# Kernel optimization log

Measured on AMD Instinct MI355X. Metric: run time of the kernel, lower is better.

## Reference

```python
import jax, jax.numpy as jnp
import numpy as np

HEADS = 8
LN_EPS = 1e-5
BN_EPS = 1e-5
MIN_EPS, MAX_EPS = 1e-4, 10.0


def _ln(x, g, b):
    m = x.mean(-1, keepdims=True)
    v = x.var(-1, keepdims=True)
    return (x - m) / jnp.sqrt(v + LN_EPS) * g + b


def _pos2d(a, b, dim, temperature=10000.0):
    # faithful to build_2d_sincos_position_embedding(w=a, h=b)
    grid_a = jnp.arange(a, dtype=jnp.float32)
    grid_b = jnp.arange(b, dtype=jnp.float32)
    ga, gb = jnp.meshgrid(grid_a, grid_b, indexing='ij')  # (a, b)
    pos_dim = dim // 4
    omega = 1.0 / (temperature ** (jnp.arange(pos_dim, dtype=jnp.float32) / pos_dim))
    out_a = ga.flatten()[:, None] * omega[None]
    out_b = gb.flatten()[:, None] * omega[None]
    return jnp.concatenate([jnp.sin(out_a), jnp.cos(out_a), jnp.sin(out_b), jnp.cos(out_b)], axis=1)  # (a*b, dim)


def _avgpool(x, k):
    bb, cc, H, W = x.shape
    return x.reshape(bb, cc, H // k, k, W // k, k).mean((3, 5))


def setup_inputs() -> dict:
    key = jax.random.key(0)
    c1, c2, bs = 256, 512, 16
    ks = jax.random.split(key, 12)

    def lin(k, o, i):
        return (jax.random.normal(k, (o, i), jnp.float32) * (1.0 / np.sqrt(i))).astype(jnp.float32)

    return {
        'a3': jax.random.normal(ks[0], (bs, c1, 80, 80), jnp.float32),
        'a4': jax.random.normal(ks[1], (bs, c2, 40, 40), jnp.float32),
        'conv_w': lin(ks[2], c1, c2), 'conv_b': jnp.zeros((c1,), jnp.float32),
        'bn_g': jnp.ones((c1,), jnp.float32), 'bn_b': jnp.zeros((c1,), jnp.float32),
        'q_w': lin(ks[3], c1, c1), 'q_b': jnp.zeros((c1,), jnp.float32),
        'q_ln_g': jnp.ones((c1,), jnp.float32), 'q_ln_b': jnp.zeros((c1,), jnp.float32),
        'k_w': lin(ks[4], c1, c1), 'k_b': jnp.zeros((c1,), jnp.float32),
        'k_ln_g': jnp.ones((c1,), jnp.float32), 'k_ln_b': jnp.zeros((c1,), jnp.float32),
        'v_w': lin(ks[5], c1, c1), 'v_b': jnp.zeros((c1,), jnp.float32),
        'out_w': lin(ks[6], c1, c1), 'out_b': jnp.zeros((c1,), jnp.float32),
        'lin1_w': lin(ks[7], 4 * c1, c1), 'lin1_b': jnp.zeros((4 * c1,), jnp.float32),
        'lin2_w': lin(ks[8], c1, 4 * c1), 'lin2_b': jnp.zeros((c1,), jnp.float32),
        'norm1_g': jnp.ones((c1,), jnp.float32), 'norm1_b': jnp.zeros((c1,), jnp.float32),
        'norm2_g': jnp.ones((c1,), jnp.float32), 'norm2_b': jnp.zeros((c1,), jnp.float32),
        'idx': 10,
    }


def reference(a3, a4, conv_w, conv_b, bn_g, bn_b, q_w, q_b, q_ln_g, q_ln_b,
              k_w, k_b, k_ln_g, k_ln_b, v_w, v_b, out_w, out_b,
              lin1_w, lin1_b, lin2_w, lin2_b, norm1_g, norm1_b, norm2_g, norm2_b, idx):
    a3 = jnp.nan_to_num(a3, nan=0.0, posinf=1e4, neginf=-1e4)
    a4 = jnp.nan_to_num(a4, nan=0.0, posinf=1e4, neginf=-1e4)
    orig_a3, orig_a4 = a3, a4

    # high_to_low_embed: 1x1 conv + BatchNorm (eval: running_mean=0, running_var=1)
    a4e = jnp.einsum('bchw,oc->bohw', a4, conv_w) + conv_b[None, :, None, None]
    a4e = a4e / jnp.sqrt(1.0 + BN_EPS) * bn_g[None, :, None, None] + bn_b[None, :, None, None]

    if idx == 10:
        a3d = _avgpool(a3, 2)
    else:
        a3d = _avgpool(a3, 4)
        a4e = _avgpool(a4e, 2)

    bs, c, h, w = a3d.shape
    tgt = h * w
    src = a4e.shape[2] * a4e.shape[3]

    residual = a3d.reshape(bs, c, tgt).transpose(0, 2, 1)      # (bs, tgt, c)
    a3f = a3d.reshape(bs, c, tgt).transpose(2, 0, 1)            # (tgt, bs, c)
    a4f = a4e.reshape(bs, c, src).transpose(2, 0, 1)            # (src, bs, c)

    pos = _pos2d(h, w, c)[:, None, :]                           # (h*w, 1, c)
    a3f = a3f + pos
    a4f = a4f + pos                                             # src == tgt by construction

    Q = jax.nn.relu(_ln(a3f @ q_w.T + q_b, q_ln_g, q_ln_b))
    K = jax.nn.relu(_ln(a4f @ k_w.T + k_b, k_ln_g, k_ln_b))
    V = a4f @ v_w.T + v_b

    hd = c // HEADS
    Q = Q.reshape(tgt, bs, HEADS, hd).transpose(1, 2, 0, 3)     # (b, h, tgt, hd)
    K = K.reshape(src, bs, HEADS, hd).transpose(1, 2, 0, 3)
    V = V.reshape(src, bs, HEADS, hd).transpose(1, 2, 0, 3)

    m = max(src, tgt)
    wi = (np.pi / 2) * jnp.arange(1, m + 1, dtype=jnp.float32) / m  # (m,)
    sq = jnp.sin(wi[:tgt])[None, None, :, None]
    cq = jnp.cos(wi[:tgt])[None, None, :, None]
    sk = jnp.sin(wi[:src])[None, None, :, None]
    ck = jnp.cos(wi[:src])[None, None, :, None]
    Q_ = jnp.concatenate([Q * sq, Q * cq], -1)                  # (b, h, tgt, 2hd)
    K_ = jnp.concatenate([K * sk, K * ck], -1)                  # (b, h, src, 2hd)

    KV = jnp.einsum('bhsd,bhse->bhde', K_, V)                   # (b, h, 2hd, hd)
    Zden = jnp.einsum('bhld,bhd->bhl', Q_, K_.sum(2))
    Z = 1.0 / jnp.clip(Zden, MIN_EPS, MAX_EPS)
    attn = jnp.einsum('bhld,bhde->bhle', Q_, KV) * Z[..., None]  # (b, h, tgt, hd)

    attn = attn.transpose(2, 0, 1, 3).reshape(tgt, bs, c)
    out = (attn @ out_w.T + out_b).transpose(1, 0, 2)           # (bs, tgt, c)
    out = _ln(out, norm1_g, norm1_b)
    out = residual + out

    res2 = out
    ff = jax.nn.gelu(out @ lin1_w.T + lin1_b, approximate=False) @ lin2_w.T + lin2_b
    ff = _ln(ff, norm2_g, norm2_b)
    out = res2 + ff

    a3_sa = out.transpose(0, 2, 1).reshape(bs, c, h, w)
    a3_sa = jax.image.resize(a3_sa, orig_a3.shape, 'bilinear')  # align_corners=False
    a3_sa = a3_sa * orig_a3

    B4, C4, H4, W4 = orig_a4.shape
    a4_up = jax.image.resize(orig_a4, (B4, C4, 2 * H4, 2 * W4), 'bilinear')
    return (a3_sa, a4_up)
```

## Files before the change

### kernel.cpp

```cpp
#include <hip/hip_runtime.h>
#include <math.h>


typedef __attribute__((ext_vector_type(8))) short bf16x8;
typedef __attribute__((ext_vector_type(8))) unsigned short us8;
typedef __attribute__((ext_vector_type(4))) unsigned short us4h;
typedef __attribute__((ext_vector_type(4))) float f32x4;

__device__ __forceinline__ unsigned short f2bf(float f) {
  unsigned int u = __float_as_uint(f);
  u += 0x7fff + ((u >> 16) & 1);
  return (unsigned short)(u >> 16);
}
__device__ __forceinline__ float bf2f(unsigned short u) {
  return __uint_as_float(((unsigned int)u) << 16);
}

__global__ __launch_bounds__(256) void wprep_kernel(
    const float* __restrict__ cw, const float* __restrict__ qw,
    const float* __restrict__ kw, const float* __restrict__ vw,
    const float* __restrict__ ow, const float* __restrict__ l1w,
    const float* __restrict__ l2w, unsigned short* __restrict__ wbf) {
  int gid = blockIdx.x * 256 + threadIdx.x;
  size_t e0 = (size_t)gid * 8;
  const float* src; size_t off;
  if (e0 < 131072)      { src = cw;  off = e0; }
  else if (e0 < 196608) { src = qw;  off = e0 - 131072; }
  else if (e0 < 262144) { src = kw;  off = e0 - 196608; }
  else if (e0 < 327680) { src = vw;  off = e0 - 262144; }
  else if (e0 < 393216) { src = ow;  off = e0 - 327680; }
  else if (e0 < 655360) { src = l1w; off = e0 - 393216; }
  else                  { src = l2w; off = e0 - 655360; }
  float4 v0 = *(const float4*)(src + off);
  float4 v1 = *(const float4*)(src + off + 4);
  us8 r;
  r[0] = f2bf(v0.x); r[1] = f2bf(v0.y); r[2] = f2bf(v0.z); r[3] = f2bf(v0.w);
  r[4] = f2bf(v1.x); r[5] = f2bf(v1.y); r[6] = f2bf(v1.z); r[7] = f2bf(v1.w);
  *(us8*)(wbf + e0) = r;
}

__global__ void pos_kernel(float* __restrict__ pos) {
  int s = blockIdx.x, c = threadIdx.x;
  int y = s / 40, x = s - y * 40;
  int quad = c >> 6, i = c & 63;
  float omega = expf(-(float)i * (9.2103403719761836f / 64.0f));
  float coord = (quad < 2) ? (float)y : (float)x;
  float a = coord * omega;
  pos[s * 256 + c] = (quad & 1) ? cosf(a) : sinf(a);
}

__global__ __launch_bounds__(640) void avgpool_kernel(
    const float* __restrict__ a3, const float* __restrict__ pos,
    unsigned short* __restrict__ X3) {
  __shared__ float buf2[256][44];
  int y = blockIdx.x, b = blockIdx.y;
  int tid = threadIdx.x;
  int x2 = tid % 20, cq = tid / 20;
#pragma unroll
  for (int it = 0; it < 8; ++it) {
    int c = cq + 32 * it;
    const float* p = a3 + (((size_t)(b * 256 + c) * 80 + 2 * y) * 80 + x2 * 4);
    float4 r0 = *(const float4*)p;
    float4 r1 = *(const float4*)(p + 80);
    buf2[c][2 * x2]     = 0.25f * ((r0.x + r0.y) + (r1.x + r1.y));
    buf2[c][2 * x2 + 1] = 0.25f * ((r0.z + r0.w) + (r1.z + r1.w));
  }
  __syncthreads();
  size_t t0 = (size_t)b * 1600 + y * 40;
  int sbase = y * 40;
#pragma unroll
  for (int it = 0; it < 4; ++it) {
    int idx = it * 640 + tid;
    int c = idx & 255, xq = idx >> 8;
    int x0 = xq * 4;
    float4 v = *(const float4*)&buf2[c][x0];
#pragma unroll
    for (int j = 0; j < 4; ++j) {
      float pv = pos[(size_t)(sbase + x0 + j) * 256 + c];
      float vv = (j == 0) ? v.x : (j == 1) ? v.y : (j == 2) ? v.z : v.w;
      X3[(t0 + x0 + j) * 256 + c] = f2bf(vv + pv);
    }
  }
}

__global__ __launch_bounds__(256) void a4t_kernel(
    const float* __restrict__ a4, unsigned short* __restrict__ a4t) {
  __shared__ float buf[64][65];
  int s0 = blockIdx.x * 64, k0 = blockIdx.y * 64, b = blockIdx.z;
  const float* src = a4 + ((size_t)b * 512 + k0) * 1600 + s0;
#pragma unroll
  for (int p = 0; p < 4; ++p) {
    int idx = p * 256 + threadIdx.x;
    int kk = idx >> 4, s4 = (idx & 15) * 4;
    float4 v = *(const float4*)(src + (size_t)kk * 1600 + s4);
    buf[kk][s4 + 0] = v.x; buf[kk][s4 + 1] = v.y;
    buf[kk][s4 + 2] = v.z; buf[kk][s4 + 3] = v.w;
  }
  __syncthreads();
  unsigned short* dst = a4t + ((size_t)b * 1600 + s0) * 512 + k0;
#pragma unroll
  for (int p = 0; p < 4; ++p) {
    int idx = p * 256 + threadIdx.x;
    int ss = idx >> 4, kq = (idx & 15) * 4;
    us4h v;
    v[0] = f2bf(buf[kq + 0][ss]); v[1] = f2bf(buf[kq + 1][ss]);
    v[2] = f2bf(buf[kq + 2][ss]); v[3] = f2bf(buf[kq + 3][ss]);
    *(us4h*)(dst + (size_t)ss * 512 + kq) = v;
  }
}

template<int EPI>
__global__ __launch_bounds__(256) void fgemm(
    const unsigned short* __restrict__ A, const unsigned short* __restrict__ W,
    const float* __restrict__ bias, void* __restrict__ outp,
    const int K, const int ldN,
    const float* __restrict__ posb,
    const float* __restrict__ g1, const float* __restrict__ b1,
    const unsigned short* __restrict__ res) {
  __shared__ __align__(16) unsigned short Albs[64][40];
  __shared__ __align__(16) unsigned short Wlds[256][40];
  __shared__ float part[2][64][2];
  int tid = threadIdx.x;
  int lane = tid & 63, w = tid >> 6;
  int m0 = (w >> 1) * 32, n0 = (w & 1) * 128;
  int g = lane >> 4, cl = lane & 15;
  int t0 = blockIdx.x * 64, o0 = blockIdx.y * 256;
  f32x4 acc[2][8] = {};
  int arr = tid >> 2, acol = (tid & 3) * 8;

  for (int k0 = 0; k0 < K; k0 += 32) {
    __syncthreads();
    *(us8*)&Albs[arr][acol] = *(const us8*)(A + (size_t)(t0 + arr) * K + (k0 + acol));
#pragma unroll
    for (int p = 0; p < 4; ++p) {
      int idx = p * 256 + tid;
      int rr = idx >> 2, cc = (idx & 3) * 8;
      *(us8*)&Wlds[rr][cc] = *(const us8*)(W + (size_t)(o0 + rr) * K + (k0 + cc));
    }
    __syncthreads();
    bf16x8 af[2], bw[8];
#pragma unroll
    for (int ms = 0; ms < 2; ++ms)
      af[ms] = *(const bf16x8*)&Albs[m0 + ms * 16 + cl][g * 8];
#pragma unroll
    for (int ns = 0; ns < 8; ++ns)
      bw[ns] = *(const bf16x8*)&Wlds[n0 + ns * 16 + cl][g * 8];
#pragma unroll
    for (int ms = 0; ms < 2; ++ms)
#pragma unroll
      for (int ns = 0; ns < 8; ++ns)
        acc[ms][ns] = __builtin_amdgcn_mfma_f32_16x16x32_bf16(af[ms], bw[ns], acc[ms][ns], 0, 0, 0);
  }

  float bv[8];
#pragma unroll
  for (int ns = 0; ns < 8; ++ns) bv[ns] = bias[o0 + n0 + ns * 16 + cl];
  int sbase = t0 % 1600;

  if constexpr (EPI == 2 || EPI == 3 || EPI == 5) {
#pragma unroll
    for (int ms = 0; ms < 2; ++ms) {
#pragma unroll
      for (int i = 0; i < 4; ++i) {
        float p = 0.f, q = 0.f;
#pragma unroll
        for (int ns = 0; ns < 8; ++ns) {
          float v = acc[ms][ns][i] + bv[ns];
          p += v; q += v * v;
        }
        p += __shfl_xor(p, 1); q += __shfl_xor(q, 1);
        p += __shfl_xor(p, 2); q += __shfl_xor(q, 2);
        p += __shfl_xor(p, 4); q += __shfl_xor(q, 4);
        p += __shfl_xor(p, 8); q += __shfl_xor(q, 8);
        if (cl == 0) {
          int rl = m0 + ms * 16 + g * 4 + i;
          part[w & 1][rl][0] = p;
          part[w & 1][rl][1] = q;
        }
      }
    }
    __syncthreads();
  }

  unsigned short* ob = (unsigned short*)outp;
  float* of = (float*)outp;
#pragma unroll
  for (int ms = 0; ms < 2; ++ms) {
#pragma unroll
    for (int i = 0; i < 4; ++i) {
      int rl = m0 + ms * 16 + g * 4 + i;
      int t = t0 + rl;
      float mean = 0.f, inv = 0.f;
      if constexpr (EPI == 2 || EPI == 3 || EPI == 5) {
        float sp = part[0][rl][0] + part[1][rl][0];
        float sq = part[0][rl][1] + part[1][rl][1];
        mean = sp * (1.f / 256.f);
        float var = sq * (1.f / 256.f) - mean * mean;
        inv = rsqrtf(var + 1e-5f);
      }
#pragma unroll
      for (int ns = 0; ns < 8; ++ns) {
        int col = n0 + ns * 16 + cl;
        float v = acc[ms][ns][i] + bv[ns];
        size_t oidx = (size_t)t * ldN + o0 + col;
        if constexpr (EPI == 0) {
          ob[oidx] = f2bf(v);
        } else if constexpr (EPI == 1) {
          const float is = 0.99999500003749968f;
          float y = v * (is * g1[col]) + b1[col] + posb[(size_t)(sbase + rl) * 256 + col];
          ob[oidx] = f2bf(y);
        } else if constexpr (EPI == 2) {
          float y = (v - mean) * inv * g1[col] + b1[col];
          ob[oidx] = f2bf(fmaxf(y, 0.f));
        } else if constexpr (EPI == 3) {
          float y = (v - mean) * inv * g1[col] + b1[col];
          y += bf2f(res[(size_t)t * 256 + col]) - posb[(size_t)(sbase + rl) * 256 + col];
          ob[oidx] = f2bf(y);
        } else if constexpr (EPI == 4) {
          float y = 0.5f * v * (1.f + erff(v * 0.7071067811865475f));
          ob[oidx] = f2bf(y);
        } else {
          float y = (v - mean) * inv * g1[col] + b1[col];
          y += bf2f(res[(size_t)t * 256 + col]);
          of[oidx] = y;
        }
      }
    }
  }
}

__global__ __launch_bounds__(256) void kv_kernel(
    const unsigned short* __restrict__ Kb, const unsigned short* __restrict__ Vb,
    float* __restrict__ KVp, float* __restrict__ Ksp) {
  __shared__ float Kc[64][32];
  __shared__ float Vc[64][32];
  __shared__ float sv[64], cv[64];
  __shared__ float red[4][64];
  int bx = blockIdx.x;
  int bh = bx / 5, sp = bx - bh * 5;
  int b = bh >> 3, h = bh & 7;
  int tid = threadIdx.x;
  int e = tid & 31, dg = tid >> 5;
  int d4 = dg * 4;
  int dks = tid & 63, partid = tid >> 6;
  float accs[4] = {0.f, 0.f, 0.f, 0.f};
  float accc[4] = {0.f, 0.f, 0.f, 0.f};
  float ks = 0.f;
  size_t base = ((size_t)b * 1600) * 256 + h * 32;
  for (int s0 = sp * 320; s0 < sp * 320 + 320; s0 += 64) {
    __syncthreads();
#pragma unroll
    for (int p = 0; p < 8; ++p) {
      int si = dg + p * 8;
      Kc[si][e] = bf2f(Kb[base + (size_t)(s0 + si) * 256 + e]);
      Vc[si][e] = bf2f(Vb[base + (size_t)(s0 + si) * 256 + e]);
    }
    if (tid < 64) {
      float wv = 1.5707963267948966f * (float)(s0 + tid + 1) * (1.0f / 1600.0f);
      sv[tid] = sinf(wv);
      cv[tid] = cosf(wv);
    }
    __syncthreads();
#pragma unroll 8
    for (int si = 0; si < 64; ++si) {
      float vv = Vc[si][e];
      float sn = sv[si], cs = cv[si];
      float4 k4 = *(const float4*)&Kc[si][d4];
      float p0 = k4.x * vv, p1 = k4.y * vv, p2 = k4.z * vv, p3 = k4.w * vv;
      accs[0] = fmaf(p0, sn, accs[0]); accc[0] = fmaf(p0, cs, accc[0]);
      accs[1] = fmaf(p1, sn, accs[1]); accc[1] = fmaf(p1, cs, accc[1]);
      accs[2] = fmaf(p2, sn, accs[2]); accc[2] = fmaf(p2, cs, accc[2]);
      accs[3] = fmaf(p3, sn, accs[3]); accc[3] = fmaf(p3, cs, accc[3]);
    }
#pragma unroll 4
    for (int q = 0; q < 16; ++q) {
      int si = partid * 16 + q;
      float kvv = (dks < 32) ? Kc[si][dks] * sv[si] : Kc[si][dks - 32] * cv[si];
      ks += kvv;
    }
  }
  red[partid][dks] = ks;
  __syncthreads();
  size_t ob = (size_t)sp * 128 + bh;
  if (tid < 64)
    Ksp[ob * 64 + tid] = (red[0][tid] + red[1][tid]) + (red[2][tid] + red[3][tid]);
#pragma unroll
  for (int i = 0; i < 4; ++i) {
    KVp[ob * 2048 + (d4 + i) * 32 + e] = accs[i];
    KVp[ob * 2048 + (32 + d4 + i) * 32 + e] = accc[i];
  }
}

__global__ __launch_bounds__(256) void kvred_kernel(
    const float* __restrict__ KVp, const float* __restrict__ Ksp,
    float* __restrict__ KV, float* __restrict__ Ks) {
  int bh = blockIdx.x, tid = threadIdx.x;
  size_t o = (size_t)bh * 2048 + tid * 8;
  float4 s0 = make_float4(0, 0, 0, 0), s1 = make_float4(0, 0, 0, 0);
#pragma unroll
  for (int sp = 0; sp < 5; ++sp) {
    const float* p = KVp + ((size_t)sp * 128 + bh) * 2048 + tid * 8;
    float4 a = *(const float4*)p;
    float4 b2 = *(const float4*)(p + 4);
    s0.x += a.x; s0.y += a.y; s0.z += a.z; s0.w += a.w;
    s1.x += b2.x; s1.y += b2.y; s1.z += b2.z; s1.w += b2.w;
  }
  *(float4*)(KV + o) = s0;
  *(float4*)(KV + o + 4) = s1;
  if (tid < 64) {
    float t = 0.f;
#pragma unroll
    for (int sp = 0; sp < 5; ++sp) t += Ksp[((size_t)sp * 128 + bh) * 64 + tid];
    Ks[bh * 64 + tid] = t;
  }
}

__global__ __launch_bounds__(256) void attn_kernel(
    const unsigned short* __restrict__ Qb, const float* __restrict__ KV,
    const float* __restrict__ Ksum, unsigned short* __restrict__ attn) {
  int grp = threadIdx.x >> 5;
  int e = threadIdx.x & 31;
  int t = blockIdx.x * 8 + grp;
  int b = t / 1600, s = t - b * 1600;
  float wv = 1.5707963267948966f * (float)(s + 1) * (1.0f / 1600.0f);
  float sq = sinf(wv), cq = cosf(wv);
  const unsigned short* qrow = Qb + (size_t)t * 256;
  for (int h = 0; h < 8; ++h) {
    int bh = b * 8 + h;
    const float* kv = KV + (size_t)bh * 2048;
    const float* ksm = Ksum + (size_t)bh * 64;
    float qe = bf2f(qrow[h * 32 + e]);
    float zp = qe * (sq * ksm[e] + cq * ksm[32 + e]);
    zp += __shfl_xor(zp, 1); zp += __shfl_xor(zp, 2);
    zp += __shfl_xor(zp, 4); zp += __shfl_xor(zp, 8); zp += __shfl_xor(zp, 16);
    float acc = 0.f;
#pragma unroll 8
    for (int d = 0; d < 32; ++d) {
      float qv = bf2f(qrow[h * 32 + d]);
      acc = fmaf(qv * sq, kv[d * 32 + e], acc);
      acc = fmaf(qv * cq, kv[(32 + d) * 32 + e], acc);
    }
    float zc = fminf(fmaxf(zp, 1e-4f), 10.0f);
    attn[(size_t)t * 256 + h * 32 + e] = f2bf(acc * (1.0f / zc));
  }
}

__global__ __launch_bounds__(256) void transpose_kernel(
    const float* __restrict__ X, float* __restrict__ Y) {
  __shared__ float buf[40 * 257];
  int y = blockIdx.x, b = blockIdx.y;
  int tid = threadIdx.x;
  size_t t0 = (size_t)b * 1600 + y * 40;
  for (int it = 0; it < 40; ++it)
    buf[it * 257 + tid] = X[(t0 + it) * 256 + tid];
  __syncthreads();
  for (int it = 0; it < 40; ++it) {
    int idx = it * 256 + tid;
    int c = idx / 40, x = idx - c * 40;
    Y[((size_t)(b * 256 + c) * 1600) + y * 40 + x] = buf[x * 257 + c];
  }
}

__device__ __forceinline__ float bilin40(const float* sm, int Y, int X) {
  float fy = Y * 0.5f - 0.25f;
  int iy = (int)floorf(fy);
  float dy = fy - (float)iy;
  int y0 = iy < 0 ? 0 : iy;
  int y1 = (iy + 1) > 39 ? 39 : (iy + 1);
  float fx = X * 0.5f - 0.25f;
  int ix = (int)floorf(fx);
  float dx = fx - (float)ix;
  int x0 = ix < 0 ? 0 : ix;
  int x1 = (ix + 1) > 39 ? 39 : (ix + 1);
  float v00 = sm[y0 * 40 + x0], v01 = sm[y0 * 40 + x1];
  float v10 = sm[y1 * 40 + x0], v11 = sm[y1 * 40 + x1];
  return (1.f - dy) * ((1.f - dx) * v00 + dx * v01) +
         dy * ((1.f - dx) * v10 + dx * v11);
}

__global__ __launch_bounds__(256) void upsample_mul_kernel(
    const float* __restrict__ src, const float* __restrict__ a3, float* __restrict__ out) {
  __shared__ float sm[1600];
  int c = blockIdx.x, b = blockIdx.y;
  size_t sbase = ((size_t)b * 256 + c) * 1600;
  for (int i = threadIdx.x; i < 1600; i += 256) sm[i] = src[sbase + i];
  __syncthreads();
  size_t obase = ((size_t)b * 256 + c) * 6400;
  for (int it = 0; it < 25; ++it) {
    int idx = it * 256 + threadIdx.x;
    int Y = idx / 80, X = idx - Y * 80;
    out[obase + idx] = bilin40(sm, Y, X) * a3[obase + idx];
  }
}

__global__ __launch_bounds__(256) void upsample_kernel(
    const float* __restrict__ src, float* __restrict__ out) {
  __shared__ float sm[1600];
  int c = blockIdx.x, b = blockIdx.y;
  size_t sbase = ((size_t)b * 512 + c) * 1600;
  for (int i = threadIdx.x; i < 1600; i += 256) sm[i] = src[sbase + i];
  __syncthreads();
  size_t obase = ((size_t)b * 512 + c) * 6400;
  for (int it = 0; it < 25; ++it) {
    int idx = it * 256 + threadIdx.x;
    int Y = idx / 80, X = idx - Y * 80;
    out[obase + idx] = bilin40(sm, Y, X);
  }
}

extern "C" void kernel_launch(void* const* d_in, const int* in_sizes, int n_in,
                              void* d_out, int out_size, void* d_ws, size_t ws_size,
                              hipStream_t stream) {
  const float* a3     = (const float*)d_in[0];
  const float* a4     = (const float*)d_in[1];
  const float* conv_w = (const float*)d_in[2];
  const float* conv_b = (const float*)d_in[3];
  const float* bn_g   = (const float*)d_in[4];
  const float* bn_b   = (const float*)d_in[5];
  const float* q_w    = (const float*)d_in[6];
  const float* q_b    = (const float*)d_in[7];
  const float* q_ln_g = (const float*)d_in[8];
  const float* q_ln_b = (const float*)d_in[9];
  const float* k_w    = (const float*)d_in[10];
  const float* k_b    = (const float*)d_in[11];
  const float* k_ln_g = (const float*)d_in[12];
  const float* k_ln_b = (const float*)d_in[13];
  const float* v_w    = (const float*)d_in[14];
  const float* v_b    = (const float*)d_in[15];
  const float* out_w  = (const float*)d_in[16];
  const float* out_b  = (const float*)d_in[17];
  const float* lin1_w = (const float*)d_in[18];
  const float* lin1_b = (const float*)d_in[19];
  const float* lin2_w = (const float*)d_in[20];
  const float* lin2_b = (const float*)d_in[21];
  const float* n1_g   = (const float*)d_in[22];
  const float* n1_b   = (const float*)d_in[23];
  const float* n2_g   = (const float*)d_in[24];
  const float* n2_b   = (const float*)d_in[25];
  (void)in_sizes; (void)n_in; (void)out_size; (void)ws_size;

  float* ws = (float*)d_ws;
  float* pos  = ws + 0;
  unsigned short* wbf = (unsigned short*)(ws + 409600);
  float* KV   = ws + 868352;
  float* Ks   = ws + 1130496;
  float* KVp  = ws + 1138688;
  float* Ksp  = ws + 2449408;
  unsigned short* X3b  = (unsigned short*)(ws + 2490368);
  unsigned short* X4b  = (unsigned short*)(ws + 5767168);
  unsigned short* Qbb  = (unsigned short*)(ws + 9043968);
  unsigned short* Kbb  = (unsigned short*)(ws + 12320768);
  unsigned short* Vbb  = (unsigned short*)(ws + 15597568);
  unsigned short* o1b  = (unsigned short*)(ws + 18874368);
  unsigned short* a4tb = (unsigned short*)(ws + 22151168);
  unsigned short* ffhb = (unsigned short*)(ws + 22151168);
  float* out2 = ws + 9043968;
  float* a3p  = ws + 15597568;

  const unsigned short* w_conv = wbf;
  const unsigned short* w_q    = wbf + 131072;
  const unsigned short* w_k    = wbf + 196608;
  const unsigned short* w_v    = wbf + 262144;
  const unsigned short* w_o    = wbf + 327680;
  const unsigned short* w_l1   = wbf + 393216;
  const unsigned short* w_l2   = wbf + 655360;

  float* out0 = (float*)d_out;
  float* out1f = out0 + (size_t)16 * 256 * 80 * 80;

  wprep_kernel<<<448, 256, 0, stream>>>(conv_w, q_w, k_w, v_w, out_w, lin1_w, lin2_w, wbf);
  pos_kernel<<<1600, 256, 0, stream>>>(pos);
  avgpool_kernel<<<dim3(40, 16), 640, 0, stream>>>(a3, pos, X3b);
  a4t_kernel<<<dim3(25, 8, 16), 256, 0, stream>>>(a4, a4tb);
  fgemm<1><<<dim3(400, 1), 256, 0, stream>>>(a4tb, w_conv, conv_b, X4b, 512, 256, pos, bn_g, bn_b, nullptr);
  fgemm<2><<<dim3(400, 1), 256, 0, stream>>>(X3b, w_q, q_b, Qbb, 256, 256, nullptr, q_ln_g, q_ln_b, nullptr);
  fgemm<2><<<dim3(400, 1), 256, 0, stream>>>(X4b, w_k, k_b, Kbb, 256, 256, nullptr, k_ln_g, k_ln_b, nullptr);
  fgemm<0><<<dim3(400, 1), 256, 0, stream>>>(X4b, w_v, v_b, Vbb, 256, 256, nullptr, nullptr, nullptr, nullptr);
  kv_kernel<<<640, 256, 0, stream>>>(Kbb, Vbb, KVp, Ksp);
  kvred_kernel<<<128, 256, 0, stream>>>(KVp, Ksp, KV, Ks);
  attn_kernel<<<3200, 256, 0, stream>>>(Qbb, KV, Ks, Kbb );
  fgemm<3><<<dim3(400, 1), 256, 0, stream>>>(Kbb, w_o, out_b, o1b, 256, 256, pos, n1_g, n1_b, X3b);
  fgemm<4><<<dim3(400, 4), 256, 0, stream>>>(o1b, w_l1, lin1_b, ffhb, 256, 1024, nullptr, nullptr, nullptr, nullptr);
  fgemm<5><<<dim3(400, 1), 256, 0, stream>>>(ffhb, w_l2, lin2_b, out2, 1024, 256, nullptr, n2_g, n2_b, o1b);
  transpose_kernel<<<dim3(40, 16), 256, 0, stream>>>(out2, a3p);
  upsample_mul_kernel<<<dim3(256, 16), 256, 0, stream>>>(a3p, a3, out0);
  upsample_kernel<<<dim3(512, 16), 256, 0, stream>>>(a4, out1f);
}
```

Baseline: 455.2 us.

## Prefetch GEMM tiles into registers, fuse QKV launches, vectorize bilinear upsample

The GEMM core now loads the next K-slice of A and W into registers while the MFMAs for the current slice run, overlapping global-load latency with compute. The three Q/K/V projection GEMMs are merged into one launch with a 3-wide grid, removing two kernel launches and letting the three projections run concurrently. The epilogue selector changes from a template parameter to a runtime argument, which can add branching and register pressure. The upsample kernels now compute four output pixels per thread using the fixed 2x bilinear weights and use float4 loads and stores, cutting index math and memory transactions.

```diff
diff --git a/kernel.cpp b/kernel.cpp
--- a/kernel.cpp
+++ b/kernel.cpp
@@ -109,47 +109,67 @@
   }
 }
 
-template<int EPI>
-__global__ __launch_bounds__(256) void fgemm(
+struct __align__(16) SmemT {
+  unsigned short Albs[64][40];
+  unsigned short Wlds[256][40];
+  float part[2][64][2];
+};
+
+__device__ __forceinline__ void gemm_core(
+    SmemT& S,
     const unsigned short* __restrict__ A, const unsigned short* __restrict__ W,
     const float* __restrict__ bias, void* __restrict__ outp,
-    const int K, const int ldN,
+    int K, int ldN, int t0, int o0, int epi,
     const float* __restrict__ posb,
     const float* __restrict__ g1, const float* __restrict__ b1,
     const unsigned short* __restrict__ res) {
-  __shared__ __align__(16) unsigned short Albs[64][40];
-  __shared__ __align__(16) unsigned short Wlds[256][40];
-  __shared__ float part[2][64][2];
   int tid = threadIdx.x;
   int lane = tid & 63, w = tid >> 6;
   int m0 = (w >> 1) * 32, n0 = (w & 1) * 128;
   int g = lane >> 4, cl = lane & 15;
-  int t0 = blockIdx.x * 64, o0 = blockIdx.y * 256;
   f32x4 acc[2][8] = {};
   int arr = tid >> 2, acol = (tid & 3) * 8;
 
+  us8 pa = *(const us8*)(A + (size_t)(t0 + arr) * K + acol);
+  us8 pw[4];
+#pragma unroll
+  for (int p = 0; p < 4; ++p) {
+    int idx = p * 256 + tid;
+    int rr = idx >> 2, cc = (idx & 3) * 8;
+    pw[p] = *(const us8*)(W + (size_t)(o0 + rr) * K + cc);
+  }
+
   for (int k0 = 0; k0 < K; k0 += 32) {
     __syncthreads();
-    *(us8*)&Albs[arr][acol] = *(const us8*)(A + (size_t)(t0 + arr) * K + (k0 + acol));
+    *(us8*)&S.Albs[arr][acol] = pa;
 #pragma unroll
     for (int p = 0; p < 4; ++p) {
       int idx = p * 256 + tid;
       int rr = idx >> 2, cc = (idx & 3) * 8;
-      *(us8*)&Wlds[rr][cc] = *(const us8*)(W + (size_t)(o0 + rr) * K + (k0 + cc));
+      *(us8*)&S.Wlds[rr][cc] = pw[p];
     }
     __syncthreads();
-    bf16x8 af[2], bw[8];
+    if (k0 + 32 < K) {
+      pa = *(const us8*)(A + (size_t)(t0 + arr) * K + (k0 + 32 + acol));
+#pragma unroll
+      for (int p = 0; p < 4; ++p) {
+        int idx = p * 256 + tid;
+        int rr = idx >> 2, cc = (idx & 3) * 8;
+        pw[p] = *(const us8*)(W + (size_t)(o0 + rr) * K + (k0 + 32 + cc));
+      }
+    }
+    bf16x8 af[2], bw8[8];
 #pragma unroll
     for (int ms = 0; ms < 2; ++ms)
-      af[ms] = *(const bf16x8*)&Albs[m0 + ms * 16 + cl][g * 8];
+      af[ms] = *(const bf16x8*)&S.Albs[m0 + ms * 16 + cl][g * 8];
 #pragma unroll
     for (int ns = 0; ns < 8; ++ns)
-      bw[ns] = *(const bf16x8*)&Wlds[n0 + ns * 16 + cl][g * 8];
+      bw8[ns] = *(const bf16x8*)&S.Wlds[n0 + ns * 16 + cl][g * 8];
 #pragma unroll
     for (int ms = 0; ms < 2; ++ms)
 #pragma unroll
       for (int ns = 0; ns < 8; ++ns)
-        acc[ms][ns] = __builtin_amdgcn_mfma_f32_16x16x32_bf16(af[ms], bw[ns], acc[ms][ns], 0, 0, 0);
+        acc[ms][ns] = __builtin_amdgcn_mfma_f32_16x16x32_bf16(af[ms], bw8[ns], acc[ms][ns], 0, 0, 0);
   }
 
   float bv[8];
@@ -157,7 +177,8 @@
   for (int ns = 0; ns < 8; ++ns) bv[ns] = bias[o0 + n0 + ns * 16 + cl];
   int sbase = t0 % 1600;
 
-  if constexpr (EPI == 2 || EPI == 3 || EPI == 5) {
+  bool needLN = (epi == 2) || (epi == 3) || (epi == 5);
+  if (needLN) {
 #pragma unroll
     for (int ms = 0; ms < 2; ++ms) {
 #pragma unroll
@@ -174,8 +195,8 @@
         p += __shfl_xor(p, 8); q += __shfl_xor(q, 8);
         if (cl == 0) {
           int rl = m0 + ms * 16 + g * 4 + i;
-          part[w & 1][rl][0] = p;
-          part[w & 1][rl][1] = q;
+          S.part[w & 1][rl][0] = p;
+          S.part[w & 1][rl][1] = q;
         }
       }
     }
@@ -191,9 +212,9 @@
       int rl = m0 + ms * 16 + g * 4 + i;
       int t = t0 + rl;
       float mean = 0.f, inv = 0.f;
-      if constexpr (EPI == 2 || EPI == 3 || EPI == 5) {
-        float sp = part[0][rl][0] + part[1][rl][0];
-        float sq = part[0][rl][1] + part[1][rl][1];
+      if (needLN) {
+        float sp = S.part[0][rl][0] + S.part[1][rl][0];
+        float sq = S.part[0][rl][1] + S.part[1][rl][1];
         mean = sp * (1.f / 256.f);
         float var = sq * (1.f / 256.f) - mean * mean;
         inv = rsqrtf(var + 1e-5f);
@@ -203,20 +224,20 @@
         int col = n0 + ns * 16 + cl;
         float v = acc[ms][ns][i] + bv[ns];
         size_t oidx = (size_t)t * ldN + o0 + col;
-        if constexpr (EPI == 0) {
+        if (epi == 0) {
           ob[oidx] = f2bf(v);
-        } else if constexpr (EPI == 1) {
+        } else if (epi == 1) {
           const float is = 0.99999500003749968f;
           float y = v * (is * g1[col]) + b1[col] + posb[(size_t)(sbase + rl) * 256 + col];
           ob[oidx] = f2bf(y);
-        } else if constexpr (EPI == 2) {
+        } else if (epi == 2) {
           float y = (v - mean) * inv * g1[col] + b1[col];
           ob[oidx] = f2bf(fmaxf(y, 0.f));
-        } else if constexpr (EPI == 3) {
+        } else if (epi == 3) {
           float y = (v - mean) * inv * g1[col] + b1[col];
           y += bf2f(res[(size_t)t * 256 + col]) - posb[(size_t)(sbase + rl) * 256 + col];
           ob[oidx] = f2bf(y);
-        } else if constexpr (EPI == 4) {
+        } else if (epi == 4) {
           float y = 0.5f * v * (1.f + erff(v * 0.7071067811865475f));
           ob[oidx] = f2bf(y);
         } else {
@@ -227,6 +248,40 @@
       }
     }
   }
+}
+
+__global__ __launch_bounds__(256) void fgemm(
+    const unsigned short* __restrict__ A, const unsigned short* __restrict__ W,
+    const float* __restrict__ bias, void* __restrict__ outp,
+    int K, int ldN, int epi,
+    const float* __restrict__ posb,
+    const float* __restrict__ g1, const float* __restrict__ b1,
+    const unsigned short* __restrict__ res) {
+  __shared__ SmemT S;
+  gemm_core(S, A, W, bias, outp, K, ldN, blockIdx.x * 64, blockIdx.y * 256, epi,
+            posb, g1, b1, res);
+}
+
+__global__ __launch_bounds__(256) void qkv_kernel(
+    const unsigned short* __restrict__ X3b, const unsigned short* __restrict__ X4b,
+    const unsigned short* __restrict__ w_q, const unsigned short* __restrict__ w_k,
+    const unsigned short* __restrict__ w_v,
+    const float* __restrict__ q_b, const float* __restrict__ k_b, const float* __restrict__ v_b,
+    const float* __restrict__ q_g, const float* __restrict__ q_bt,
+    const float* __restrict__ k_g, const float* __restrict__ k_bt,
+    unsigned short* __restrict__ Qo, unsigned short* __restrict__ Ko,
+    unsigned short* __restrict__ Vo) {
+  __shared__ SmemT S;
+  int grp = blockIdx.y;
+  const unsigned short* A = (grp == 0) ? X3b : X4b;
+  const unsigned short* W = (grp == 0) ? w_q : (grp == 1 ? w_k : w_v);
+  const float* bias = (grp == 0) ? q_b : (grp == 1 ? k_b : v_b);
+  const float* g1 = (grp == 0) ? q_g : k_g;
+  const float* b1 = (grp == 0) ? q_bt : k_bt;
+  void* out = (grp == 0) ? (void*)Qo : (grp == 1 ? (void*)Ko : (void*)Vo);
+  int epi = (grp == 2) ? 0 : 2;
+  gemm_core(S, A, W, bias, out, 256, 256, blockIdx.x * 64, 0, epi,
+            nullptr, g1, b1, nullptr);
 }
 
 __global__ __launch_bounds__(256) void kv_kernel(
@@ -361,21 +416,27 @@
   }
 }
 
-__device__ __forceinline__ float bilin40(const float* sm, int Y, int X) {
+__device__ __forceinline__ float4 up_row4(const float* sm, int Y, int q) {
   float fy = Y * 0.5f - 0.25f;
   int iy = (int)floorf(fy);
   float dy = fy - (float)iy;
   int y0 = iy < 0 ? 0 : iy;
   int y1 = (iy + 1) > 39 ? 39 : (iy + 1);
-  float fx = X * 0.5f - 0.25f;
-  int ix = (int)floorf(fx);
-  float dx = fx - (float)ix;
-  int x0 = ix < 0 ? 0 : ix;
-  int x1 = (ix + 1) > 39 ? 39 : (ix + 1);
-  float v00 = sm[y0 * 40 + x0], v01 = sm[y0 * 40 + x1];
-  float v10 = sm[y1 * 40 + x0], v11 = sm[y1 * 40 + x1];
-  return (1.f - dy) * ((1.f - dx) * v00 + dx * v01) +
-         dy * ((1.f - dx) * v10 + dx * v11);
+  const float* r0 = sm + y0 * 40;
+  const float* r1 = sm + y1 * 40;
+  int cm1 = (2 * q - 1) < 0 ? 0 : (2 * q - 1);
+  int cp2 = (2 * q + 2) > 39 ? 39 : (2 * q + 2);
+  float w1 = 1.f - dy;
+  float s0 = w1 * r0[cm1]       + dy * r1[cm1];
+  float s1 = w1 * r0[2 * q]     + dy * r1[2 * q];
+  float s2 = w1 * r0[2 * q + 1] + dy * r1[2 * q + 1];
+  float s3 = w1 * r0[cp2]       + dy * r1[cp2];
+  float4 o;
+  o.x = 0.25f * s0 + 0.75f * s1;
+  o.y = 0.75f * s1 + 0.25f * s2;
+  o.z = 0.25f * s1 + 0.75f * s2;
+  o.w = 0.75f * s2 + 0.25f * s3;
+  return o;
 }
 
 __global__ __launch_bounds__(256) void upsample_mul_kernel(
@@ -383,13 +444,16 @@
   __shared__ float sm[1600];
   int c = blockIdx.x, b = blockIdx.y;
   size_t sbase = ((size_t)b * 256 + c) * 1600;
-  for (int i = threadIdx.x; i < 1600; i += 256) sm[i] = src[sbase + i];
+  for (int i = threadIdx.x; i < 400; i += 256)
+    *(float4*)&sm[i * 4] = *(const float4*)(src + sbase + i * 4);
   __syncthreads();
   size_t obase = ((size_t)b * 256 + c) * 6400;
-  for (int it = 0; it < 25; ++it) {
-    int idx = it * 256 + threadIdx.x;
-    int Y = idx / 80, X = idx - Y * 80;
-    out[obase + idx] = bilin40(sm, Y, X) * a3[obase + idx];
+  for (int i = threadIdx.x; i < 1600; i += 256) {
+    int Y = i / 20, q = i - Y * 20;
+    float4 o = up_row4(sm, Y, q);
+    float4 m = *(const float4*)(a3 + obase + i * 4);
+    o.x *= m.x; o.y *= m.y; o.z *= m.z; o.w *= m.w;
+    *(float4*)(out + obase + i * 4) = o;
   }
 }
 
@@ -398,13 +462,14 @@
   __shared__ float sm[1600];
   int c = blockIdx.x, b = blockIdx.y;
   size_t sbase = ((size_t)b * 512 + c) * 1600;
-  for (int i = threadIdx.x; i < 1600; i += 256) sm[i] = src[sbase + i];
+  for (int i = threadIdx.x; i < 400; i += 256)
+    *(float4*)&sm[i * 4] = *(const float4*)(src + sbase + i * 4);
   __syncthreads();
   size_t obase = ((size_t)b * 512 + c) * 6400;
-  for (int it = 0; it < 25; ++it) {
-    int idx = it * 256 + threadIdx.x;
-    int Y = idx / 80, X = idx - Y * 80;
-    out[obase + idx] = bilin40(sm, Y, X);
+  for (int i = threadIdx.x; i < 1600; i += 256) {
+    int Y = i / 20, q = i - Y * 20;
+    float4 o = up_row4(sm, Y, q);
+    *(float4*)(out + obase + i * 4) = o;
   }
 }
 
@@ -472,16 +537,15 @@
   pos_kernel<<<1600, 256, 0, stream>>>(pos);
   avgpool_kernel<<<dim3(40, 16), 640, 0, stream>>>(a3, pos, X3b);
   a4t_kernel<<<dim3(25, 8, 16), 256, 0, stream>>>(a4, a4tb);
-  fgemm<1><<<dim3(400, 1), 256, 0, stream>>>(a4tb, w_conv, conv_b, X4b, 512, 256, pos, bn_g, bn_b, nullptr);
-  fgemm<2><<<dim3(400, 1), 256, 0, stream>>>(X3b, w_q, q_b, Qbb, 256, 256, nullptr, q_ln_g, q_ln_b, nullptr);
-  fgemm<2><<<dim3(400, 1), 256, 0, stream>>>(X4b, w_k, k_b, Kbb, 256, 256, nullptr, k_ln_g, k_ln_b, nullptr);
-  fgemm<0><<<dim3(400, 1), 256, 0, stream>>>(X4b, w_v, v_b, Vbb, 256, 256, nullptr, nullptr, nullptr, nullptr);
+  fgemm<<<dim3(400, 1), 256, 0, stream>>>(a4tb, w_conv, conv_b, X4b, 512, 256, 1, pos, bn_g, bn_b, nullptr);
+  qkv_kernel<<<dim3(400, 3), 256, 0, stream>>>(X3b, X4b, w_q, w_k, w_v,
+      q_b, k_b, v_b, q_ln_g, q_ln_b, k_ln_g, k_ln_b, Qbb, Kbb, Vbb);
   kv_kernel<<<640, 256, 0, stream>>>(Kbb, Vbb, KVp, Ksp);
   kvred_kernel<<<128, 256, 0, stream>>>(KVp, Ksp, KV, Ks);
   attn_kernel<<<3200, 256, 0, stream>>>(Qbb, KV, Ks, Kbb );
-  fgemm<3><<<dim3(400, 1), 256, 0, stream>>>(Kbb, w_o, out_b, o1b, 256, 256, pos, n1_g, n1_b, X3b);
-  fgemm<4><<<dim3(400, 4), 256, 0, stream>>>(o1b, w_l1, lin1_b, ffhb, 256, 1024, nullptr, nullptr, nullptr, nullptr);
-  fgemm<5><<<dim3(400, 1), 256, 0, stream>>>(ffhb, w_l2, lin2_b, out2, 1024, 256, nullptr, n2_g, n2_b, o1b);
+  fgemm<<<dim3(400, 1), 256, 0, stream>>>(Kbb, w_o, out_b, o1b, 256, 256, 3, pos, n1_g, n1_b, X3b);
+  fgemm<<<dim3(400, 4), 256, 0, stream>>>(o1b, w_l1, lin1_b, ffhb, 256, 1024, 4, nullptr, nullptr, nullptr, nullptr);
+  fgemm<<<dim3(400, 1), 256, 0, stream>>>(ffhb, w_l2, lin2_b, out2, 1024, 256, 5, nullptr, n2_g, n2_b, o1b);
   transpose_kernel<<<dim3(40, 16), 256, 0, stream>>>(out2, a3p);
   upsample_mul_kernel<<<dim3(256, 16), 256, 0, stream>>>(a3p, a3, out0);
   upsample_kernel<<<dim3(512, 16), 256, 0, stream>>>(a4, out1f);
```

Measured after the change: 513.6 us. 1.13x slower.
